# Optimization experiments

Hardware: AMD Instinct MI355X
Metric: run time of the kernel (lower is better)

The kernel has to match this reference:

```python
import jax, jax.numpy as jnp
import numpy as np

# Winograd F(4x4, 3x3) transform matrices (m=4, r=3, a=6)
B_T = jnp.array([[4.,0.,-5.,0.,1.,0.],
                 [0.,-4.,-4.,1.,1.,0.],
                 [0.,4.,-4.,-1.,1.,0.],
                 [0.,-2.,-1.,2.,1.,0.],
                 [0.,2.,-1.,-2.,1.,0.],
                 [0.,4.,0.,-5.,0.,1.]], dtype=jnp.float32)
G = jnp.array([[1/4.,0.,0.],
               [-1/6.,-1/6.,-1/6.],
               [-1/6.,1/6.,-1/6.],
               [1/24.,1/12.,1/6.],
               [1/24.,-1/12.,1/6.],
               [0.,0.,1.]], dtype=jnp.float32)
A_T = jnp.array([[1.,1.,1.,1.,1.,0.],
                 [0.,1.,-1.,2.,-2.,0.],
                 [0.,1.,1.,4.,4.,0.],
                 [0.,1.,-1.,8.,-8.,1.]], dtype=jnp.float32)

M_OUT, R_K, A_IN = 4, 3, 6  # output tile m, kernel r, input tile a = m+r-1


def setup_inputs() -> dict:
    key = jax.random.key(0)
    k1, k2 = jax.random.split(key)
    x = jax.random.normal(k1, (16, 64, 130, 130), dtype=jnp.float32)
    w = jax.random.normal(k2, (64, 64, 3, 3), dtype=jnp.float32) * 0.05
    return {"input": x, "weight": w}


def reference(input, weight):
    N, C, H, W = input.shape
    K = weight.shape[0]
    m, r, a = M_OUT, R_K, A_IN
    T = (H - r + 1) // m  # tiles per spatial dim (perfect tiling)

    # Filter transform: U[k,c] = G @ w[k,c] @ G^T  -> [K,C,a,a]
    U = jnp.einsum('ai,kcij,bj->kcab', G, weight, G)

    # Extract overlapping a x a input tiles with stride m: [N,C,T,a,T,a]
    idx = (jnp.arange(T) * m)[:, None] + jnp.arange(a)[None, :]  # [T,a]
    tiles = input[:, :, idx, :][:, :, :, :, idx]

    # Input transform: V = B^T @ tile @ B  -> [N,T,T,C,a,a]
    V = jnp.einsum('ai,nctisj,bj->ntscab', B_T, tiles, B_T)
    Vp = V.reshape(N * T * T, C, a, a)  # [P,C,a,a]

    # Elementwise (tile-domain) multiply + channel reduce: M[p,k] = sum_c U[k,c]*V[p,c]
    Mt = jnp.einsum('kcab,pcab->pkab', U, Vp)  # [P,K,a,a]

    # Output transform: Y_tile = A^T @ M @ A -> [P,K,m,m]
    Yt = jnp.einsum('ai,pkij,bj->pkab', A_T, Mt, A_T)

    out = T * m  # = H - r + 1
    Y = Yt.reshape(N, T, T, K, m, m).transpose(0, 3, 1, 4, 2, 5).reshape(N, K, out, out)
    return Y
```

## Files before the change

### kernel.cpp

```cpp
#include <hip/hip_runtime.h>


__constant__ float c_AT[24] = {
  1.f, 0.f, 0.f, 0.f,
  1.f, 1.f, 1.f, 1.f,
  1.f,-1.f, 1.f,-1.f,
  1.f, 2.f, 4.f, 8.f,
  1.f,-2.f, 4.f,-8.f,
  0.f, 0.f, 0.f, 1.f
};

__global__ __launch_bounds__(256) void k_filter(const float* __restrict__ w,
                                                float* __restrict__ U) {
  int g = blockIdx.x * 256 + threadIdx.x;
  int k = g & 63;
  int c = g >> 6;
  const float* wp = w + (size_t)(k * 64 + c) * 9;
  float w00 = wp[0], w01 = wp[1], w02 = wp[2];
  float w10 = wp[3], w11 = wp[4], w12 = wp[5];
  float w20 = wp[6], w21 = wp[7], w22 = wp[8];
  const float G[6][3] = {
    {0.25f, 0.f, 0.f},
    {-1.f/6.f, -1.f/6.f, -1.f/6.f},
    {-1.f/6.f,  1.f/6.f, -1.f/6.f},
    {1.f/24.f,  1.f/12.f, 1.f/6.f},
    {1.f/24.f, -1.f/12.f, 1.f/6.f},
    {0.f, 0.f, 1.f}
  };
  float t[6][3];
#pragma unroll
  for (int a = 0; a < 6; ++a) {
    t[a][0] = G[a][0]*w00 + G[a][1]*w10 + G[a][2]*w20;
    t[a][1] = G[a][0]*w01 + G[a][1]*w11 + G[a][2]*w21;
    t[a][2] = G[a][0]*w02 + G[a][1]*w12 + G[a][2]*w22;
  }
#pragma unroll
  for (int a = 0; a < 6; ++a) {
#pragma unroll
    for (int b = 0; b < 6; ++b) {
      float u = G[b][0]*t[a][0] + G[b][1]*t[a][1] + G[b][2]*t[a][2];
      U[(size_t)(a*6+b)*4096 + c*64 + k] = u;
    }
  }
}

__global__ __launch_bounds__(256) void k_input(const float* __restrict__ x,
                                               float* __restrict__ V,
                                               int n0, int Pchunk) {
  __shared__ float Ls[34*133];
  const int tid  = threadIdx.x;
  const int bi   = blockIdx.x;
  const int band = bi & 3;
  const int c    = (bi >> 2) & 63;
  const int nl   = bi >> 8;
  const float* xp = x + (size_t)((n0 + nl) * 64 + c) * (130*130) + band * 32 * 130;
  for (int i = tid; i < 34*130; i += 256) {
    int r = i / 130;
    int col = i - r * 130;
    Ls[r*133 + col] = xp[i];
  }
  __syncthreads();
  const int tyl = tid >> 5;
  const int tx  = tid & 31;
  const int ty  = band * 8 + tyl;
  const int p   = (nl * 32 + ty) * 32 + tx;
  const float* bl = &Ls[(tyl*4)*133 + tx*4];
  float t1[6][6];
#pragma unroll
  for (int j = 0; j < 6; ++j) {
    float d0 = bl[0*133+j], d1 = bl[1*133+j], d2 = bl[2*133+j];
    float d3 = bl[3*133+j], d4 = bl[4*133+j], d5 = bl[5*133+j];
    t1[0][j] =  4.f*d0 - 5.f*d2 + d4;
    t1[1][j] = -4.f*d1 - 4.f*d2 + d3 + d4;
    t1[2][j] =  4.f*d1 - 4.f*d2 - d3 + d4;
    t1[3][j] = -2.f*d1 -     d2 + 2.f*d3 + d4;
    t1[4][j] =  2.f*d1 -     d2 - 2.f*d3 + d4;
    t1[5][j] =  4.f*d1 - 5.f*d3 + d5;
  }
  float* vb = V + (size_t)c * Pchunk + p;
  const size_t abs_ = (size_t)64 * Pchunk;
#pragma unroll
  for (int a = 0; a < 6; ++a) {
    float s0=t1[a][0], s1=t1[a][1], s2=t1[a][2], s3=t1[a][3], s4=t1[a][4], s5=t1[a][5];
    float v0 =  4.f*s0 - 5.f*s2 + s4;
    float v1 = -4.f*s1 - 4.f*s2 + s3 + s4;
    float v2 =  4.f*s1 - 4.f*s2 - s3 + s4;
    float v3 = -2.f*s1 -     s2 + 2.f*s3 + s4;
    float v4 =  2.f*s1 -     s2 - 2.f*s3 + s4;
    float v5 =  4.f*s1 - 5.f*s3 + s5;
    vb[(size_t)(a*6+0)*abs_] = v0;
    vb[(size_t)(a*6+1)*abs_] = v1;
    vb[(size_t)(a*6+2)*abs_] = v2;
    vb[(size_t)(a*6+3)*abs_] = v3;
    vb[(size_t)(a*6+4)*abs_] = v4;
    vb[(size_t)(a*6+5)*abs_] = v5;
  }
}

__global__ __launch_bounds__(256, 2) void k_gemm(const float* __restrict__ V,
                                                 const float* __restrict__ U,
                                                 float* __restrict__ out,
                                                 int n0, int Pchunk) {
  __shared__ float Vs[64*32];
  __shared__ float Us[64*64];
  const int tid = threadIdx.x;
  const int wg  = blockIdx.x;
  const int nl  = wg >> 5;
  const int ty  = wg & 31;
  const int p0  = wg * 32;
  const int pp  = tid & 15;
  const int k0  = (tid >> 4) * 4;

  const int vrow = tid >> 2;
  const int vcol = (tid & 3) * 4;
  const float* Vg = V + (size_t)vrow * Pchunk + p0 + vcol;
  const size_t abstride = (size_t)64 * Pchunk;

  float Y[2][4][4][4];
#pragma unroll
  for (int pi = 0; pi < 2; ++pi)
#pragma unroll
    for (int ki = 0; ki < 4; ++ki)
#pragma unroll
      for (int u = 0; u < 4; ++u)
#pragma unroll
        for (int v = 0; v < 4; ++v) Y[pi][ki][u][v] = 0.f;

  for (int i = 0; i < 6; ++i) {
    float au[4] = {c_AT[i*4+0], c_AT[i*4+1], c_AT[i*4+2], c_AT[i*4+3]};
    float R[2][4][4];
#pragma unroll
    for (int pi = 0; pi < 2; ++pi)
#pragma unroll
      for (int ki = 0; ki < 4; ++ki)
#pragma unroll
        for (int v = 0; v < 4; ++v) R[pi][ki][v] = 0.f;

    for (int j = 0; j < 6; ++j) {
      const int ab = i*6 + j;
      __syncthreads();
      const float* vg = Vg + (size_t)ab * abstride;
      float4 va = *(const float4*)(vg);
      float4 vb = *(const float4*)(vg + 16);
      *(float4*)(&Vs[vrow*32 + vcol])      = va;
      *(float4*)(&Vs[vrow*32 + vcol + 16]) = vb;
      const float4* ug = (const float4*)(U + (size_t)ab * 4096);
      float4* us = (float4*)Us;
      us[tid]       = ug[tid];
      us[tid + 256] = ug[tid + 256];
      us[tid + 512] = ug[tid + 512];
      us[tid + 768] = ug[tid + 768];
      __syncthreads();

      float m[2][4];
#pragma unroll
      for (int ki = 0; ki < 4; ++ki) { m[0][ki] = 0.f; m[1][ki] = 0.f; }
#pragma unroll 8
      for (int c = 0; c < 64; ++c) {
        float vA = Vs[c*32 + pp];
        float vB = Vs[c*32 + pp + 16];
        const float4 u4 = *(const float4*)(&Us[c*64 + k0]);
        float uu[4] = {u4.x, u4.y, u4.z, u4.w};
#pragma unroll
        for (int ki = 0; ki < 4; ++ki) {
          m[0][ki] += vA * uu[ki];
          m[1][ki] += vB * uu[ki];
        }
      }
      float av[4] = {c_AT[j*4+0], c_AT[j*4+1], c_AT[j*4+2], c_AT[j*4+3]};
#pragma unroll
      for (int pi = 0; pi < 2; ++pi)
#pragma unroll
        for (int ki = 0; ki < 4; ++ki)
#pragma unroll
          for (int v = 0; v < 4; ++v) R[pi][ki][v] += m[pi][ki] * av[v];
    }
#pragma unroll
    for (int pi = 0; pi < 2; ++pi)
#pragma unroll
      for (int ki = 0; ki < 4; ++ki)
#pragma unroll
        for (int u = 0; u < 4; ++u)
#pragma unroll
          for (int v = 0; v < 4; ++v) Y[pi][ki][u][v] += au[u] * R[pi][ki][v];
  }

  const int ng = n0 + nl;
#pragma unroll
  for (int pi = 0; pi < 2; ++pi) {
    const int tx = pp + pi*16;
#pragma unroll
    for (int ki = 0; ki < 4; ++ki) {
      const int k = k0 + ki;
      float* ob = out + ((size_t)(ng*64 + k)*128 + ty*4) * 128 + tx*4;
#pragma unroll
      for (int u = 0; u < 4; ++u) {
        float4 st = make_float4(Y[pi][ki][u][0], Y[pi][ki][u][1],
                                Y[pi][ki][u][2], Y[pi][ki][u][3]);
        *(float4*)(ob + (size_t)u * 128) = st;
      }
    }
  }
}

extern "C" void kernel_launch(void* const* d_in, const int* in_sizes, int n_in,
                              void* d_out, int out_size, void* d_ws, size_t ws_size,
                              hipStream_t stream) {
  const float* x = (const float*)d_in[0];
  const float* w = (const float*)d_in[1];
  float* out = (float*)d_out;
  float* U = (float*)d_ws;
  const size_t U_bytes = 36ull * 64 * 64 * 4;
  float* V = (float*)((char*)d_ws + U_bytes);
  const size_t per_n = 36ull * 1024 * 64 * 4;
  size_t avail = ws_size > U_bytes ? ws_size - U_bytes : 0;
  int chunk = (int)(avail / per_n);
  if (chunk < 1) return;
  if (chunk > 16) chunk = 16;

  k_filter<<<16, 256, 0, stream>>>(w, U);
  for (int n0 = 0; n0 < 16; n0 += chunk) {
    int cn = (16 - n0) < chunk ? (16 - n0) : chunk;
    int Pchunk = cn * 1024;
    k_input<<<cn*256, 256, 0, stream>>>(x, V, n0, Pchunk);
    k_gemm <<<cn*32,  256, 0, stream>>>(V, U, out, n0, Pchunk);
  }
}
```

Baseline: 275.0 us.

## Split Winograd GEMM into batched per-element GEMM plus separate output-transform kernel

Result: faster. 268.6 us (-2.3%).

```diff
diff --git a/kernel.cpp b/kernel.cpp
--- a/kernel.cpp
+++ b/kernel.cpp
@@ -9,6 +9,11 @@
   1.f,-2.f, 4.f,-8.f,
   0.f, 0.f, 0.f, 1.f
 };
+
+__device__ __forceinline__ void gl2lds16(const float* g, float* l) {
+  __builtin_amdgcn_global_load_lds((const __attribute__((address_space(1))) void*)g,
+                                   (__attribute__((address_space(3))) void*)l, 16, 0, 0);
+}
 
 __global__ __launch_bounds__(256) void k_filter(const float* __restrict__ w,
                                                 float* __restrict__ U) {
@@ -47,29 +52,29 @@
 __global__ __launch_bounds__(256) void k_input(const float* __restrict__ x,
                                                float* __restrict__ V,
                                                int n0, int Pchunk) {
-  __shared__ float Ls[34*133];
+  __shared__ float Ls[34*134];
   const int tid  = threadIdx.x;
   const int bi   = blockIdx.x;
   const int band = bi & 3;
   const int c    = (bi >> 2) & 63;
   const int nl   = bi >> 8;
   const float* xp = x + (size_t)((n0 + nl) * 64 + c) * (130*130) + band * 32 * 130;
-  for (int i = tid; i < 34*130; i += 256) {
-    int r = i / 130;
-    int col = i - r * 130;
-    Ls[r*133 + col] = xp[i];
+  for (int idx = tid; idx < 34*65; idx += 256) {
+    int r  = idx / 65;
+    int c2 = idx - r * 65;
+    *(float2*)&Ls[r*134 + c2*2] = *(const float2*)(xp + r*130 + c2*2);
   }
   __syncthreads();
   const int tyl = tid >> 5;
   const int tx  = tid & 31;
   const int ty  = band * 8 + tyl;
   const int p   = (nl * 32 + ty) * 32 + tx;
-  const float* bl = &Ls[(tyl*4)*133 + tx*4];
+  const float* bl = &Ls[(tyl*4)*134 + tx*4];
   float t1[6][6];
 #pragma unroll
   for (int j = 0; j < 6; ++j) {
-    float d0 = bl[0*133+j], d1 = bl[1*133+j], d2 = bl[2*133+j];
-    float d3 = bl[3*133+j], d4 = bl[4*133+j], d5 = bl[5*133+j];
+    float d0 = bl[0*134+j], d1 = bl[1*134+j], d2 = bl[2*134+j];
+    float d3 = bl[3*134+j], d4 = bl[4*134+j], d5 = bl[5*134+j];
     t1[0][j] =  4.f*d0 - 5.f*d2 + d4;
     t1[1][j] = -4.f*d1 - 4.f*d2 + d3 + d4;
     t1[2][j] =  4.f*d1 - 4.f*d2 - d3 + d4;
@@ -97,110 +102,110 @@
   }
 }
 
-__global__ __launch_bounds__(256, 2) void k_gemm(const float* __restrict__ V,
-                                                 const float* __restrict__ U,
-                                                 float* __restrict__ out,
-                                                 int n0, int Pchunk) {
-  __shared__ float Vs[64*32];
+__global__ __launch_bounds__(256) void k_gemm2(const float* __restrict__ V,
+                                               const float* __restrict__ U,
+                                               float* __restrict__ M,
+                                               int Pchunk, int nPB) {
+  __shared__ float Vs[64*256];
   __shared__ float Us[64*64];
-  const int tid = threadIdx.x;
-  const int wg  = blockIdx.x;
-  const int nl  = wg >> 5;
-  const int ty  = wg & 31;
-  const int p0  = wg * 32;
-  const int pp  = tid & 15;
-  const int k0  = (tid >> 4) * 4;
-
-  const int vrow = tid >> 2;
-  const int vcol = (tid & 3) * 4;
-  const float* Vg = V + (size_t)vrow * Pchunk + p0 + vcol;
+  const int tid  = threadIdx.x;
+  const int lane = tid & 63;
+  const int wv   = tid >> 6;
+  const unsigned bx = blockIdx.x;
+  const int ab = bx / (unsigned)nPB;
+  const int pb = bx - ab * nPB;
+  const int p0 = pb * 256;
+
+  const float* Vab = V + (size_t)ab * 64 * Pchunk + p0;
+  const float* Uab = U + (size_t)ab * 4096;
+
+#pragma unroll
+  for (int i = 0; i < 16; ++i) {
+    int r = wv + i * 4;
+    gl2lds16(Vab + (size_t)r * Pchunk + lane * 4, &Vs[r * 256]);
+  }
+#pragma unroll
+  for (int i = 0; i < 4; ++i) {
+    int li = wv + i * 4;
+    gl2lds16(Uab + li * 256 + lane * 4, &Us[li * 256]);
+  }
+  __syncthreads();
+
+  const int pt = tid & 31;
+  const int kt = tid >> 5;
+  float acc[8][8];
+#pragma unroll
+  for (int ki = 0; ki < 8; ++ki)
+#pragma unroll
+    for (int pi = 0; pi < 8; ++pi) acc[ki][pi] = 0.f;
+
+#pragma unroll 4
+  for (int c = 0; c < 64; ++c) {
+    const float4 va = *(const float4*)&Vs[c*256 + pt*4];
+    const float4 vb = *(const float4*)&Vs[c*256 + 128 + pt*4];
+    const float4 ua = *(const float4*)&Us[c*64 + kt*8];
+    const float4 ub = *(const float4*)&Us[c*64 + kt*8 + 4];
+    const float vv[8] = {va.x, va.y, va.z, va.w, vb.x, vb.y, vb.z, vb.w};
+    const float uu[8] = {ua.x, ua.y, ua.z, ua.w, ub.x, ub.y, ub.z, ub.w};
+#pragma unroll
+    for (int ki = 0; ki < 8; ++ki)
+#pragma unroll
+      for (int pi = 0; pi < 8; ++pi)
+        acc[ki][pi] += uu[ki] * vv[pi];
+  }
+
+#pragma unroll
+  for (int ki = 0; ki < 8; ++ki) {
+    float* mb = M + ((size_t)ab * 64 + kt*8 + ki) * Pchunk + p0;
+    *(float4*)(mb + pt*4)       = make_float4(acc[ki][0], acc[ki][1], acc[ki][2], acc[ki][3]);
+    *(float4*)(mb + 128 + pt*4) = make_float4(acc[ki][4], acc[ki][5], acc[ki][6], acc[ki][7]);
+  }
+}
+
+__global__ __launch_bounds__(256) void k_out(const float* __restrict__ M,
+                                             float* __restrict__ out,
+                                             int n0, int Pchunk, int bpk) {
+  const unsigned bx = blockIdx.x;
+  const int k    = bx / (unsigned)bpk;
+  const int pblk = bx - k * bpk;
+  const int p    = pblk * 256 + threadIdx.x;
+  const int nl = p >> 10;
+  const int ty = (p >> 5) & 31;
+  const int tx = p & 31;
+
+  const float* mp = M + (size_t)k * Pchunk + p;
   const size_t abstride = (size_t)64 * Pchunk;
-
-  float Y[2][4][4][4];
-#pragma unroll
-  for (int pi = 0; pi < 2; ++pi)
-#pragma unroll
-    for (int ki = 0; ki < 4; ++ki)
-#pragma unroll
-      for (int u = 0; u < 4; ++u)
-#pragma unroll
-        for (int v = 0; v < 4; ++v) Y[pi][ki][u][v] = 0.f;
-
+  float m[36];
+#pragma unroll
+  for (int ab = 0; ab < 36; ++ab) m[ab] = mp[(size_t)ab * abstride];
+
+  float Y[4][4];
+#pragma unroll
+  for (int u = 0; u < 4; ++u)
+#pragma unroll
+    for (int v = 0; v < 4; ++v) Y[u][v] = 0.f;
+
+#pragma unroll
   for (int i = 0; i < 6; ++i) {
-    float au[4] = {c_AT[i*4+0], c_AT[i*4+1], c_AT[i*4+2], c_AT[i*4+3]};
-    float R[2][4][4];
-#pragma unroll
-    for (int pi = 0; pi < 2; ++pi)
-#pragma unroll
-      for (int ki = 0; ki < 4; ++ki)
-#pragma unroll
-        for (int v = 0; v < 4; ++v) R[pi][ki][v] = 0.f;
-
+    float R[4] = {0.f, 0.f, 0.f, 0.f};
+#pragma unroll
     for (int j = 0; j < 6; ++j) {
-      const int ab = i*6 + j;
-      __syncthreads();
-      const float* vg = Vg + (size_t)ab * abstride;
-      float4 va = *(const float4*)(vg);
-      float4 vb = *(const float4*)(vg + 16);
-      *(float4*)(&Vs[vrow*32 + vcol])      = va;
-      *(float4*)(&Vs[vrow*32 + vcol + 16]) = vb;
-      const float4* ug = (const float4*)(U + (size_t)ab * 4096);
-      float4* us = (float4*)Us;
-      us[tid]       = ug[tid];
-      us[tid + 256] = ug[tid + 256];
-      us[tid + 512] = ug[tid + 512];
-      us[tid + 768] = ug[tid + 768];
-      __syncthreads();
-
-      float m[2][4];
-#pragma unroll
-      for (int ki = 0; ki < 4; ++ki) { m[0][ki] = 0.f; m[1][ki] = 0.f; }
-#pragma unroll 8
-      for (int c = 0; c < 64; ++c) {
-        float vA = Vs[c*32 + pp];
-        float vB = Vs[c*32 + pp + 16];
-        const float4 u4 = *(const float4*)(&Us[c*64 + k0]);
-        float uu[4] = {u4.x, u4.y, u4.z, u4.w};
-#pragma unroll
-        for (int ki = 0; ki < 4; ++ki) {
-          m[0][ki] += vA * uu[ki];
-          m[1][ki] += vB * uu[ki];
-        }
-      }
-      float av[4] = {c_AT[j*4+0], c_AT[j*4+1], c_AT[j*4+2], c_AT[j*4+3]};
-#pragma unroll
-      for (int pi = 0; pi < 2; ++pi)
-#pragma unroll
-        for (int ki = 0; ki < 4; ++ki)
-#pragma unroll
-          for (int v = 0; v < 4; ++v) R[pi][ki][v] += m[pi][ki] * av[v];
+      float mm = m[i*6 + j];
+#pragma unroll
+      for (int v = 0; v < 4; ++v) R[v] += c_AT[j*4 + v] * mm;
     }
 #pragma unroll
-    for (int pi = 0; pi < 2; ++pi)
-#pragma unroll
-      for (int ki = 0; ki < 4; ++ki)
-#pragma unroll
-        for (int u = 0; u < 4; ++u)
-#pragma unroll
-          for (int v = 0; v < 4; ++v) Y[pi][ki][u][v] += au[u] * R[pi][ki][v];
-  }
-
-  const int ng = n0 + nl;
-#pragma unroll
-  for (int pi = 0; pi < 2; ++pi) {
-    const int tx = pp + pi*16;
-#pragma unroll
-    for (int ki = 0; ki < 4; ++ki) {
-      const int k = k0 + ki;
-      float* ob = out + ((size_t)(ng*64 + k)*128 + ty*4) * 128 + tx*4;
-#pragma unroll
-      for (int u = 0; u < 4; ++u) {
-        float4 st = make_float4(Y[pi][ki][u][0], Y[pi][ki][u][1],
-                                Y[pi][ki][u][2], Y[pi][ki][u][3]);
-        *(float4*)(ob + (size_t)u * 128) = st;
-      }
+    for (int u = 0; u < 4; ++u) {
+      float au = c_AT[i*4 + u];
+#pragma unroll
+      for (int v = 0; v < 4; ++v) Y[u][v] += au * R[v];
     }
   }
+
+  float* ob = out + ((size_t)((n0 + nl) * 64 + k) * 128 + ty*4) * 128 + tx*4;
+#pragma unroll
+  for (int u = 0; u < 4; ++u)
+    *(float4*)(ob + (size_t)u * 128) = make_float4(Y[u][0], Y[u][1], Y[u][2], Y[u][3]);
 }
 
 extern "C" void kernel_launch(void* const* d_in, const int* in_sizes, int n_in,
@@ -211,8 +216,7 @@
   float* out = (float*)d_out;
   float* U = (float*)d_ws;
   const size_t U_bytes = 36ull * 64 * 64 * 4;
-  float* V = (float*)((char*)d_ws + U_bytes);
-  const size_t per_n = 36ull * 1024 * 64 * 4;
+  const size_t per_n = 2ull * 36 * 1024 * 64 * 4;
   size_t avail = ws_size > U_bytes ? ws_size - U_bytes : 0;
   int chunk = (int)(avail / per_n);
   if (chunk < 1) return;
@@ -222,7 +226,11 @@
   for (int n0 = 0; n0 < 16; n0 += chunk) {
     int cn = (16 - n0) < chunk ? (16 - n0) : chunk;
     int Pchunk = cn * 1024;
-    k_input<<<cn*256, 256, 0, stream>>>(x, V, n0, Pchunk);
-    k_gemm <<<cn*32,  256, 0, stream>>>(V, U, out, n0, Pchunk);
-  }
-}
+    float* V = (float*)((char*)d_ws + U_bytes);
+    float* M = V + (size_t)36 * 64 * Pchunk;
+    int nPB = cn * 4;
+    k_input<<<cn*256,  256, 0, stream>>>(x, V, n0, Pchunk);
+    k_gemm2<<<36*nPB,  256, 0, stream>>>(V, U, M, Pchunk, nPB);
+    k_out  <<<64*nPB,  256, 0, stream>>>(M, out, n0, Pchunk, nPB);
+  }
+}
```
